# Kernel tuning notes

Hardware: AMD Instinct MI355X
Metric: run time of the kernel (lower is better)

## Reference

```python
import jax, jax.numpy as jnp
import numpy as np

N_NODES = 100000
N_EDGES = 1600000
D_IN = 128
D_HID = 128


def gcn_conv(x, src, dst, W, b, n_nodes):
    """PyG-style GCNConv: out = D^{-1/2} (A + I) D^{-1/2} (x @ W) + b.

    src/dst already include self-loops.
    """
    deg = jax.ops.segment_sum(jnp.ones_like(src, dtype=x.dtype), dst,
                              num_segments=n_nodes)
    dinv = jnp.where(deg > 0, deg ** -0.5, 0.0)
    norm = dinv[src] * dinv[dst]              # [E]
    h = x @ W                                  # [N, d_out]
    msg = h[src] * norm[:, None]               # gather + scale, [E, d_out]
    out = jax.ops.segment_sum(msg, dst, num_segments=n_nodes)
    return out + b


def setup_inputs() -> dict:
    key = jax.random.key(0)
    k1, k2, k3, k4 = jax.random.split(key, 4)
    x = jax.random.normal(k1, (N_NODES, D_IN), dtype=jnp.float32)
    edge_index = jax.random.randint(k2, (2, N_EDGES), 0, N_NODES, dtype=jnp.int64)
    s1 = (1.0 / np.sqrt(D_IN)).astype(np.float32)
    s2 = (1.0 / np.sqrt(D_HID)).astype(np.float32)
    W1 = jax.random.normal(k3, (D_IN, D_HID), dtype=jnp.float32) * s1
    b1 = jnp.zeros((D_HID,), dtype=jnp.float32)
    W2 = jax.random.normal(k4, (D_HID, D_HID), dtype=jnp.float32) * s2
    b2 = jnp.zeros((D_HID,), dtype=jnp.float32)
    return {"x": x, "edge_index": edge_index, "W1": W1, "b1": b1,
            "W2": W2, "b2": b2}


def reference(x, edge_index, W1, b1, W2, b2):
    n_nodes = x.shape[0]
    loops = jnp.arange(n_nodes, dtype=edge_index.dtype)
    src = jnp.concatenate([edge_index[0], loops])  # self-loops, as PyG default
    dst = jnp.concatenate([edge_index[1], loops])
    h = gcn_conv(x, src, dst, W1, b1, n_nodes)
    h = gcn_conv(h, src, dst, W2, b2, n_nodes)
    return h
```

## Files before the change

### kernel.cpp

```cpp
#include <hip/hip_runtime.h>

#define N_NODES 100000
#define N_EDGES 1600000

#define NBIN 196
#define BINCAP 9216
#define NPB 4096
#define EPT 16
#define BPT 36
#define PBLK ((N_EDGES + NPB - 1) / NPB)

typedef unsigned int uint;
typedef unsigned short u16;
typedef __attribute__((ext_vector_type(8))) short bf16x8;
typedef __attribute__((ext_vector_type(4))) float f32x4;

__device__ __forceinline__ uint bf16_rtne(float f) {
  uint u = __float_as_uint(f);
  return (u + 0x7fffu + ((u >> 16) & 1u)) >> 16;
}


__global__ __launch_bounds__(256) void k_zerobc(int* __restrict__ bin_cur) {
  if (threadIdx.x < NBIN) bin_cur[threadIdx.x] = 0;
}

__global__ __launch_bounds__(256) void k_part(const int* __restrict__ ei, int* __restrict__ bin_cur,
                                              uint* __restrict__ stage) {
  __shared__ uint hist[4][NBIN];
  __shared__ uint wbase[4][NBIN];
  __shared__ uint lcur[4][NBIN];
  const int t = threadIdx.x;
  const int w = t >> 6;
  const int e0 = blockIdx.x * NPB;
  for (int i = t; i < 4 * NBIN; i += 256) { (&hist[0][0])[i] = 0; (&lcur[0][0])[i] = 0; }
  __syncthreads();
  uint d[EPT];
#pragma unroll
  for (int j = 0; j < EPT; ++j) {
    int e = e0 + j * 256 + t;
    d[j] = (e < N_EDGES) ? (uint)ei[N_EDGES + e] : 0xFFFFFFFFu;
    if (d[j] != 0xFFFFFFFFu) atomicAdd(&hist[w][d[j] >> 9], 1u);
  }
  __syncthreads();
  if (t < NBIN) {
    uint h0 = hist[0][t], h1 = hist[1][t], h2 = hist[2][t], h3 = hist[3][t];
    uint tot = h0 + h1 + h2 + h3;
    uint g = tot ? (uint)atomicAdd(&bin_cur[t], (int)tot) : 0u;
    wbase[0][t] = g;
    wbase[1][t] = g + h0;
    wbase[2][t] = g + h0 + h1;
    wbase[3][t] = g + h0 + h1 + h2;
  }
  __syncthreads();
#pragma unroll
  for (int j = 0; j < EPT; ++j) {
    if (d[j] != 0xFFFFFFFFu) {
      int e = e0 + j * 256 + t;
      uint s = (uint)ei[e];
      uint b = d[j] >> 9;
      uint pos = wbase[w][b] + atomicAdd(&lcur[w][b], 1u);
      if (pos < BINCAP)
        stage[(size_t)b * BINCAP + pos] = s | ((d[j] & 511u) << 17);
    }
  }
}

__global__ __launch_bounds__(256) void k_binscan(const int* __restrict__ bin_cur,
                                                 int* __restrict__ ebase, int* __restrict__ rowptr) {
  __shared__ int sd[256];
  const int t = threadIdx.x;
  int v = (t < NBIN) ? min(bin_cur[t], BINCAP) : 0;
  int s = v;
  sd[t] = s;
  __syncthreads();
  for (int off = 1; off < 256; off <<= 1) {
    int a = (t >= off) ? sd[t - off] : 0;
    __syncthreads();
    sd[t] += a;
    __syncthreads();
  }
  if (t < NBIN) ebase[t] = sd[t] - v;
  if (t == 255) rowptr[N_NODES] = sd[255];
}

__global__ __launch_bounds__(256) void k_bin2(const int* __restrict__ bin_cur, const uint* __restrict__ stage,
                                              const int* __restrict__ ebase,
                                              float* __restrict__ dinv, int* __restrict__ rowptr,
                                              int* __restrict__ ep) {
  __shared__ int cnt[512];
  __shared__ int sd[256];
  __shared__ int curs[512];
  const int b = blockIdx.x, t = threadIdx.x;
  cnt[t] = 0; cnt[t + 256] = 0;
  __syncthreads();
  const int n = min(bin_cur[b], BINCAP);
  const uint* sb = stage + (size_t)b * BINCAP;
  uint r[BPT];
#pragma unroll
  for (int j = 0; j < BPT; ++j) {
    int i = j * 256 + t;
    r[j] = (i < n) ? sb[i] : 0xFFFFFFFFu;
  }
#pragma unroll
  for (int j = 0; j < BPT; ++j)
    if (r[j] != 0xFFFFFFFFu) atomicAdd(&cnt[r[j] >> 17], 1);
  __syncthreads();
  int v0 = cnt[t * 2], v1 = cnt[t * 2 + 1];
  int s = v0 + v1;
  sd[t] = s;
  __syncthreads();
  for (int off = 1; off < 256; off <<= 1) {
    int a = (t >= off) ? sd[t - off] : 0;
    __syncthreads();
    sd[t] += a;
    __syncthreads();
  }
  int run = sd[t] - s;
  int eb = ebase[b];
  int c0 = eb + run, c1 = eb + run + v0;
  int g0 = b * 512 + t * 2;
  if (g0 < N_NODES) {
    rowptr[g0] = c0;
    dinv[g0] = rsqrtf((float)(v0 + 1));
  }
  if (g0 + 1 < N_NODES) {
    rowptr[g0 + 1] = c1;
    dinv[g0 + 1] = rsqrtf((float)(v1 + 1));
  }
  curs[t * 2] = c0; curs[t * 2 + 1] = c1;
  __syncthreads();
#pragma unroll
  for (int j = 0; j < BPT; ++j)
    if (r[j] != 0xFFFFFFFFu) {
      int pos = atomicAdd(&curs[r[j] >> 17], 1);
      ep[pos] = (int)(r[j] & 0x1FFFFu);
    }
}


__global__ __launch_bounds__(256) void k_prepw(const float* __restrict__ W1, const float* __restrict__ W2,
                                               uint* __restrict__ S1, uint* __restrict__ S2) {
  int u = blockIdx.x * 256 + threadIdx.x;
  const float* W = blockIdx.y ? W2 : W1;
  uint* S = blockIdx.y ? S2 : S1;
  int lane = u & 63;
  int kcnt = u >> 6;
  int kc = kcnt & 3;
  int nt = kcnt >> 2;
  int n = nt * 16 + (lane & 15);
  int k0 = kc * 32 + (lane >> 4) * 8;
  float f[8];
#pragma unroll
  for (int j = 0; j < 8; ++j) f[j] = W[(size_t)(k0 + j) * 128 + n];
  uint4 pk;
  pk.x = bf16_rtne(f[0]) | (bf16_rtne(f[1]) << 16);
  pk.y = bf16_rtne(f[2]) | (bf16_rtne(f[3]) << 16);
  pk.z = bf16_rtne(f[4]) | (bf16_rtne(f[5]) << 16);
  pk.w = bf16_rtne(f[6]) | (bf16_rtne(f[7]) << 16);
  ((uint4*)S)[u] = pk;
}


__global__ __launch_bounds__(256) void k_gemm(const void* __restrict__ Ain, int a_f32,
                                              const uint* __restrict__ Wsw,
                                              u16* __restrict__ OutH, int nrows) {
  __shared__ uint As[4096];
  __shared__ uint Bs[8192];
  const int tid = threadIdx.x;
  const int R = blockIdx.x * 64;
  {
    const uint4* src = (const uint4*)Wsw;
    uint4* dst = (uint4*)Bs;
#pragma unroll
    for (int v = 0; v < 8; ++v) dst[tid + v * 256] = src[tid + v * 256];
  }
  const int unit = tid & 15;
  const int kc_s = unit >> 2;
  const int quad_s = unit & 3;
#pragma unroll
  for (int pass = 0; pass < 4; ++pass) {
    int row = pass * 16 + (tid >> 4);
    int gr = R + row;
    if (gr >= nrows) gr = nrows - 1;
    uint4 pk;
    if (a_f32) {
      const float* srcr = (const float*)Ain + (size_t)gr * 128 + unit * 8;
      float4 f0 = ((const float4*)srcr)[0];
      float4 f1 = ((const float4*)srcr)[1];
      pk.x = bf16_rtne(f0.x) | (bf16_rtne(f0.y) << 16);
      pk.y = bf16_rtne(f0.z) | (bf16_rtne(f0.w) << 16);
      pk.z = bf16_rtne(f1.x) | (bf16_rtne(f1.y) << 16);
      pk.w = bf16_rtne(f1.z) | (bf16_rtne(f1.w) << 16);
    } else {
      pk = ((const uint4*)((const uint*)Ain + (size_t)gr * 64))[unit];
    }
    int lane_t = quad_s * 16 + (row & 15);
    *(uint4*)&As[((pass * 4 + kc_s) * 64 + lane_t) * 4] = pk;
  }
  __syncthreads();

  const int w = tid >> 6;
  const int lane = tid & 63;
  bf16x8 a0 = *(bf16x8*)&As[((w * 4 + 0) * 64 + lane) * 4];
  bf16x8 a1 = *(bf16x8*)&As[((w * 4 + 1) * 64 + lane) * 4];
  bf16x8 a2 = *(bf16x8*)&As[((w * 4 + 2) * 64 + lane) * 4];
  bf16x8 a3 = *(bf16x8*)&As[((w * 4 + 3) * 64 + lane) * 4];
  f32x4 acc[8];
#pragma unroll
  for (int nt = 0; nt < 8; ++nt) acc[nt] = (f32x4){0.f, 0.f, 0.f, 0.f};
#pragma unroll
  for (int nt = 0; nt < 8; ++nt) {
    bf16x8 b0 = *(bf16x8*)&Bs[((nt * 4 + 0) * 64 + lane) * 4];
    bf16x8 b1 = *(bf16x8*)&Bs[((nt * 4 + 1) * 64 + lane) * 4];
    bf16x8 b2 = *(bf16x8*)&Bs[((nt * 4 + 2) * 64 + lane) * 4];
    bf16x8 b3 = *(bf16x8*)&Bs[((nt * 4 + 3) * 64 + lane) * 4];
    acc[nt] = __builtin_amdgcn_mfma_f32_16x16x32_bf16(a0, b0, acc[nt], 0, 0, 0);
    acc[nt] = __builtin_amdgcn_mfma_f32_16x16x32_bf16(a1, b1, acc[nt], 0, 0, 0);
    acc[nt] = __builtin_amdgcn_mfma_f32_16x16x32_bf16(a2, b2, acc[nt], 0, 0, 0);
    acc[nt] = __builtin_amdgcn_mfma_f32_16x16x32_bf16(a3, b3, acc[nt], 0, 0, 0);
  }
  const int colb = lane & 15;
  const int quad = lane >> 4;
#pragma unroll
  for (int nt = 0; nt < 8; ++nt) {
#pragma unroll
    for (int r = 0; r < 4; ++r) {
      int gr = R + w * 16 + quad * 4 + r;
      if (gr < nrows)
        OutH[(size_t)gr * 128 + nt * 16 + colb] = (u16)bf16_rtne(acc[nt][r]);
    }
  }
}


__device__ __forceinline__ void bacc(float& ax, float& ay, uint v, float w) {
  ax += w * __uint_as_float(v << 16);
  ay += w * __uint_as_float(v & 0xffff0000u);
}

__device__ __forceinline__ void agg_node(const uint* __restrict__ hb, const float* __restrict__ dinv,
                                         const int* __restrict__ ep, int node, int lane,
                                         int beg, int end, float dn, float& ax, float& ay) {
  uint selfv = hb[(size_t)node * 64 + lane];
  bacc(ax, ay, selfv, dn);
  int e = beg;
  for (; e + 8 <= end; e += 8) {
    int p[8];
#pragma unroll
    for (int j = 0; j < 8; ++j) p[j] = ep[e + j];
    float wt[8];
#pragma unroll
    for (int j = 0; j < 8; ++j) wt[j] = dinv[p[j]];
    uint v[8];
#pragma unroll
    for (int j = 0; j < 8; ++j) v[j] = hb[(size_t)p[j] * 64 + lane];
#pragma unroll
    for (int j = 0; j < 8; ++j) bacc(ax, ay, v[j], wt[j]);
  }
  if (e + 4 <= end) {
    int p[4];
#pragma unroll
    for (int j = 0; j < 4; ++j) p[j] = ep[e + j];
    float wt[4];
#pragma unroll
    for (int j = 0; j < 4; ++j) wt[j] = dinv[p[j]];
    uint v[4];
#pragma unroll
    for (int j = 0; j < 4; ++j) v[j] = hb[(size_t)p[j] * 64 + lane];
#pragma unroll
    for (int j = 0; j < 4; ++j) bacc(ax, ay, v[j], wt[j]);
    e += 4;
  }
  for (; e < end; ++e) {
    int p = ep[e];
    float wt = dinv[p];
    uint v = hb[(size_t)p * 64 + lane];
    bacc(ax, ay, v, wt);
  }
}


__global__ __launch_bounds__(256) void k_aggm(const uint* __restrict__ hb, const float* __restrict__ dinv,
                                              const int* __restrict__ rowptr, const int* __restrict__ ep,
                                              const float* __restrict__ bias, const uint* __restrict__ Wsw,
                                              u16* __restrict__ outH) {
  __shared__ uint Abf[16 * 64];
  const int w = threadIdx.x >> 6;
  const int lane = threadIdx.x & 63;
  const int nb = blockIdx.x * 16;
#pragma unroll 1
  for (int j = 0; j < 4; ++j) {
    const int lr = w * 4 + j;
    const int node = nb + lr;
    const int beg = rowptr[node];
    const int end = rowptr[node + 1];
    const float dn = dinv[node];
    float ax = 0.f, ay = 0.f;
    agg_node(hb, dinv, ep, node, lane, beg, end, dn, ax, ay);
    int c = lane * 2;
    float rx = dn * ax + bias[c];
    float ry = dn * ay + bias[c + 1];
    uint pk = bf16_rtne(rx) | (bf16_rtne(ry) << 16);
    Abf[(lr * 64 + lane) ^ ((lr & 7) << 2)] = pk;
  }
  __syncthreads();
  const int row = lane & 15;
  const int kq = lane >> 4;
  bf16x8 a[4];
#pragma unroll
  for (int kc = 0; kc < 4; ++kc) {
    int ui = row * 64 + kc * 16 + kq * 4;
    a[kc] = *(bf16x8*)&Abf[ui ^ ((row & 7) << 2)];
  }
  const int colb = lane & 15;
  const int quad = lane >> 4;
#pragma unroll
  for (int nt2 = 0; nt2 < 2; ++nt2) {
    const int nt = w * 2 + nt2;
    f32x4 acc = (f32x4){0.f, 0.f, 0.f, 0.f};
#pragma unroll
    for (int kc = 0; kc < 4; ++kc) {
      bf16x8 bfr = *(const bf16x8*)((const uint4*)Wsw + (nt * 4 + kc) * 64 + lane);
      acc = __builtin_amdgcn_mfma_f32_16x16x32_bf16(a[kc], bfr, acc, 0, 0, 0);
    }
#pragma unroll
    for (int r2 = 0; r2 < 4; ++r2) {
      int gr = nb + quad * 4 + r2;
      outH[(size_t)gr * 128 + nt * 16 + colb] = (u16)bf16_rtne(acc[r2]);
    }
  }
}


__global__ __launch_bounds__(256) void k_agg(const uint* __restrict__ hb, const float* __restrict__ dinv,
                                             const int* __restrict__ rowptr, const int* __restrict__ ep,
                                             const float* __restrict__ bias,
                                             float* __restrict__ outf) {
  int wid = threadIdx.x >> 6;
  int lane = threadIdx.x & 63;
  int node = blockIdx.x * 4 + wid;
  if (node >= N_NODES) return;
  int beg = rowptr[node];
  int end = rowptr[node + 1];
  float dn = dinv[node];
  float ax = 0.f, ay = 0.f;
  agg_node(hb, dinv, ep, node, lane, beg, end, dn, ax, ay);
  int c = lane * 2;
  float2 o;
  o.x = dn * ax + bias[c];
  o.y = dn * ay + bias[c + 1];
  *(float2*)(outf + (size_t)node * 128 + c) = o;
}


extern "C" void kernel_launch(void* const* d_in, const int* in_sizes, int n_in,
                              void* d_out, int out_size, void* d_ws, size_t ws_size,
                              hipStream_t stream) {
  const float* x  = (const float*)d_in[0];
  const int*   ei = (const int*)d_in[1];
  const float* W1 = (const float*)d_in[2];
  const float* b1 = (const float*)d_in[3];
  const float* W2 = (const float*)d_in[4];
  const float* b2 = (const float*)d_in[5];
  float* out = (float*)d_out;

  char* p = (char*)d_ws;
  uint*  hb     = (uint*)p;  p += (size_t)N_NODES * 64 * sizeof(uint);
  int*   ep     = (int*)p;   p += (size_t)N_EDGES * sizeof(int);
  uint*  wsw1   = (uint*)p;  p += 8192 * sizeof(uint);
  uint*  wsw2   = (uint*)p;  p += 8192 * sizeof(uint);
  float* dinv   = (float*)p; p += (size_t)N_NODES * sizeof(float);
  int*   rowptr = (int*)p;   p += (size_t)(N_NODES + 1) * sizeof(int);
  int*   bin_cur= (int*)p;   p += (size_t)NBIN * sizeof(int);
  int*   ebase  = (int*)p;   p += (size_t)NBIN * sizeof(int);
  p = (char*)(((uintptr_t)p + 63) & ~(uintptr_t)63);
  uint*  stage  = (uint*)p;
  uint*  hb2    = (uint*)p;

  const int GG = (N_NODES + 63) / 64;

  k_zerobc<<<1, 256, 0, stream>>>(bin_cur);
  k_part<<<PBLK, 256, 0, stream>>>(ei, bin_cur, stage);
  k_binscan<<<1, 256, 0, stream>>>(bin_cur, ebase, rowptr);
  k_bin2<<<NBIN, 256, 0, stream>>>(bin_cur, stage, ebase, dinv, rowptr, ep);
  k_prepw<<<dim3(8, 2), 256, 0, stream>>>(W1, W2, wsw1, wsw2);

  k_gemm<<<GG, 256, 0, stream>>>(x, 1, wsw1, (u16*)hb, N_NODES);
  k_aggm<<<N_NODES / 16, 256, 0, stream>>>(hb, dinv, rowptr, ep, b1, wsw2, (u16*)hb2);
  k_agg<<<(N_NODES + 3) / 4, 256, 0, stream>>>(hb2, dinv, rowptr, ep, b2, out);
}
```

Before: 319.0 us.

## Pack per-edge source dinv into edge list and use nontemporal loads/stores

Edge list becomes int2 pairs of (src index, dinv[src]), filled by a new k_epw kernel after binning. Both aggregation passes then skip the dependent gather of dinv per edge. Edge pairs are read, and outputs written, with nontemporal hints so they pollute the cache less. The trade is an extra kernel pass and twice the edge-array traffic in exchange for removing a random dependent load in the hot gather loops.

```diff
diff --git a/kernel.cpp b/kernel.cpp
--- a/kernel.cpp
+++ b/kernel.cpp
@@ -12,6 +12,7 @@
 
 typedef unsigned int uint;
 typedef unsigned short u16;
+typedef unsigned long long u64;
 typedef __attribute__((ext_vector_type(8))) short bf16x8;
 typedef __attribute__((ext_vector_type(4))) float f32x4;
 
@@ -87,7 +88,7 @@
 __global__ __launch_bounds__(256) void k_bin2(const int* __restrict__ bin_cur, const uint* __restrict__ stage,
                                               const int* __restrict__ ebase,
                                               float* __restrict__ dinv, int* __restrict__ rowptr,
-                                              int* __restrict__ ep) {
+                                              int2* __restrict__ ep) {
   __shared__ int cnt[512];
   __shared__ int sd[256];
   __shared__ int curs[512];
@@ -134,8 +135,18 @@
   for (int j = 0; j < BPT; ++j)
     if (r[j] != 0xFFFFFFFFu) {
       int pos = atomicAdd(&curs[r[j] >> 17], 1);
-      ep[pos] = (int)(r[j] & 0x1FFFFu);
-    }
+      int2 pr; pr.x = (int)(r[j] & 0x1FFFFu); pr.y = 0;
+      ep[pos] = pr;
+    }
+}
+
+__global__ __launch_bounds__(256) void k_epw(int2* __restrict__ ep, const float* __restrict__ dinv) {
+  int i = blockIdx.x * 256 + threadIdx.x;
+  if (i < N_EDGES) {
+    int2 v = ep[i];
+    v.y = __float_as_int(dinv[v.x]);
+    ep[i] = v;
+  }
 }
 
 
@@ -239,50 +250,47 @@
   ay += w * __uint_as_float(v & 0xffff0000u);
 }
 
-__device__ __forceinline__ void agg_node(const uint* __restrict__ hb, const float* __restrict__ dinv,
-                                         const int* __restrict__ ep, int node, int lane,
+__device__ __forceinline__ u64 nt_ld_pair(const int2* p) {
+  return __builtin_nontemporal_load((const u64*)p);
+}
+
+__device__ __forceinline__ void agg_node(const uint* __restrict__ hb, const int2* __restrict__ ep,
+                                         int node, int lane,
                                          int beg, int end, float dn, float& ax, float& ay) {
   uint selfv = hb[(size_t)node * 64 + lane];
   bacc(ax, ay, selfv, dn);
   int e = beg;
   for (; e + 8 <= end; e += 8) {
-    int p[8];
-#pragma unroll
-    for (int j = 0; j < 8; ++j) p[j] = ep[e + j];
-    float wt[8];
-#pragma unroll
-    for (int j = 0; j < 8; ++j) wt[j] = dinv[p[j]];
+    u64 p[8];
+#pragma unroll
+    for (int j = 0; j < 8; ++j) p[j] = nt_ld_pair(&ep[e + j]);
     uint v[8];
 #pragma unroll
-    for (int j = 0; j < 8; ++j) v[j] = hb[(size_t)p[j] * 64 + lane];
-#pragma unroll
-    for (int j = 0; j < 8; ++j) bacc(ax, ay, v[j], wt[j]);
+    for (int j = 0; j < 8; ++j) v[j] = hb[(size_t)(uint)p[j] * 64 + lane];
+#pragma unroll
+    for (int j = 0; j < 8; ++j) bacc(ax, ay, v[j], __uint_as_float((uint)(p[j] >> 32)));
   }
   if (e + 4 <= end) {
-    int p[4];
-#pragma unroll
-    for (int j = 0; j < 4; ++j) p[j] = ep[e + j];
-    float wt[4];
-#pragma unroll
-    for (int j = 0; j < 4; ++j) wt[j] = dinv[p[j]];
+    u64 p[4];
+#pragma unroll
+    for (int j = 0; j < 4; ++j) p[j] = nt_ld_pair(&ep[e + j]);
     uint v[4];
 #pragma unroll
-    for (int j = 0; j < 4; ++j) v[j] = hb[(size_t)p[j] * 64 + lane];
-#pragma unroll
-    for (int j = 0; j < 4; ++j) bacc(ax, ay, v[j], wt[j]);
+    for (int j = 0; j < 4; ++j) v[j] = hb[(size_t)(uint)p[j] * 64 + lane];
+#pragma unroll
+    for (int j = 0; j < 4; ++j) bacc(ax, ay, v[j], __uint_as_float((uint)(p[j] >> 32)));
     e += 4;
   }
   for (; e < end; ++e) {
-    int p = ep[e];
-    float wt = dinv[p];
-    uint v = hb[(size_t)p * 64 + lane];
-    bacc(ax, ay, v, wt);
+    u64 p = nt_ld_pair(&ep[e]);
+    uint v = hb[(size_t)(uint)p * 64 + lane];
+    bacc(ax, ay, v, __uint_as_float((uint)(p >> 32)));
   }
 }
 
 
 __global__ __launch_bounds__(256) void k_aggm(const uint* __restrict__ hb, const float* __restrict__ dinv,
-                                              const int* __restrict__ rowptr, const int* __restrict__ ep,
+                                              const int* __restrict__ rowptr, const int2* __restrict__ ep,
                                               const float* __restrict__ bias, const uint* __restrict__ Wsw,
                                               u16* __restrict__ outH) {
   __shared__ uint Abf[16 * 64];
@@ -297,7 +305,7 @@
     const int end = rowptr[node + 1];
     const float dn = dinv[node];
     float ax = 0.f, ay = 0.f;
-    agg_node(hb, dinv, ep, node, lane, beg, end, dn, ax, ay);
+    agg_node(hb, ep, node, lane, beg, end, dn, ax, ay);
     int c = lane * 2;
     float rx = dn * ax + bias[c];
     float ry = dn * ay + bias[c + 1];
@@ -327,14 +335,15 @@
 #pragma unroll
     for (int r2 = 0; r2 < 4; ++r2) {
       int gr = nb + quad * 4 + r2;
-      outH[(size_t)gr * 128 + nt * 16 + colb] = (u16)bf16_rtne(acc[r2]);
+      __builtin_nontemporal_store((u16)bf16_rtne(acc[r2]),
+                                  outH + (size_t)gr * 128 + nt * 16 + colb);
     }
   }
 }
 
 
 __global__ __launch_bounds__(256) void k_agg(const uint* __restrict__ hb, const float* __restrict__ dinv,
-                                             const int* __restrict__ rowptr, const int* __restrict__ ep,
+                                             const int* __restrict__ rowptr, const int2* __restrict__ ep,
                                              const float* __restrict__ bias,
                                              float* __restrict__ outf) {
   int wid = threadIdx.x >> 6;
@@ -345,12 +354,13 @@
   int end = rowptr[node + 1];
   float dn = dinv[node];
   float ax = 0.f, ay = 0.f;
-  agg_node(hb, dinv, ep, node, lane, beg, end, dn, ax, ay);
+  agg_node(hb, ep, node, lane, beg, end, dn, ax, ay);
   int c = lane * 2;
-  float2 o;
-  o.x = dn * ax + bias[c];
-  o.y = dn * ay + bias[c + 1];
-  *(float2*)(outf + (size_t)node * 128 + c) = o;
+  long long ov;
+  float rx = dn * ax + bias[c];
+  float ry = dn * ay + bias[c + 1];
+  ov = (long long)(((u64)__float_as_uint(ry) << 32) | (u64)__float_as_uint(rx));
+  __builtin_nontemporal_store(ov, (long long*)(outf + (size_t)node * 128 + c));
 }
 
 
@@ -367,7 +377,7 @@
 
   char* p = (char*)d_ws;
   uint*  hb     = (uint*)p;  p += (size_t)N_NODES * 64 * sizeof(uint);
-  int*   ep     = (int*)p;   p += (size_t)N_EDGES * sizeof(int);
+  int2*  ep     = (int2*)p;  p += (size_t)N_EDGES * sizeof(int2);
   uint*  wsw1   = (uint*)p;  p += 8192 * sizeof(uint);
   uint*  wsw2   = (uint*)p;  p += 8192 * sizeof(uint);
   float* dinv   = (float*)p; p += (size_t)N_NODES * sizeof(float);
@@ -384,6 +394,7 @@
   k_part<<<PBLK, 256, 0, stream>>>(ei, bin_cur, stage);
   k_binscan<<<1, 256, 0, stream>>>(bin_cur, ebase, rowptr);
   k_bin2<<<NBIN, 256, 0, stream>>>(bin_cur, stage, ebase, dinv, rowptr, ep);
+  k_epw<<<(N_EDGES + 255) / 256, 256, 0, stream>>>(ep, dinv);
   k_prepw<<<dim3(8, 2), 256, 0, stream>>>(W1, W2, wsw1, wsw2);
 
   k_gemm<<<GG, 256, 0, stream>>>(x, 1, wsw1, (u16*)hb, N_NODES);
```

Result: slower. 361.3 us (+13.3%).

## Merge partition and first GEMM into one launch and fold small kernels

Applied to the files above, without the earlier changes.

Edge partitioning and the layer-1 GEMM now run as one grid, with blocks branching by index, so the two independent stages overlap on the device. The bin counter reset moves into the weight-prep kernel, and the bin prefix scan is recomputed inside each k_bin2 block, which drops three small launches. This trades fewer launch gaps and better occupancy for a larger shared-memory footprint in the combined kernel and a redundant scan in every bin block.

```diff
diff --git a/kernel.cpp b/kernel.cpp
--- a/kernel.cpp
+++ b/kernel.cpp
@@ -9,9 +9,11 @@
 #define EPT 16
 #define BPT 36
 #define PBLK ((N_EDGES + NPB - 1) / NPB)
+#define GG ((N_NODES + 63) / 64)
 
 typedef unsigned int uint;
 typedef unsigned short u16;
+typedef unsigned long long u64;
 typedef __attribute__((ext_vector_type(8))) short bf16x8;
 typedef __attribute__((ext_vector_type(4))) float f32x4;
 
@@ -21,126 +23,10 @@
 }
 
 
-__global__ __launch_bounds__(256) void k_zerobc(int* __restrict__ bin_cur) {
-  if (threadIdx.x < NBIN) bin_cur[threadIdx.x] = 0;
-}
-
-__global__ __launch_bounds__(256) void k_part(const int* __restrict__ ei, int* __restrict__ bin_cur,
-                                              uint* __restrict__ stage) {
-  __shared__ uint hist[4][NBIN];
-  __shared__ uint wbase[4][NBIN];
-  __shared__ uint lcur[4][NBIN];
-  const int t = threadIdx.x;
-  const int w = t >> 6;
-  const int e0 = blockIdx.x * NPB;
-  for (int i = t; i < 4 * NBIN; i += 256) { (&hist[0][0])[i] = 0; (&lcur[0][0])[i] = 0; }
-  __syncthreads();
-  uint d[EPT];
-#pragma unroll
-  for (int j = 0; j < EPT; ++j) {
-    int e = e0 + j * 256 + t;
-    d[j] = (e < N_EDGES) ? (uint)ei[N_EDGES + e] : 0xFFFFFFFFu;
-    if (d[j] != 0xFFFFFFFFu) atomicAdd(&hist[w][d[j] >> 9], 1u);
-  }
-  __syncthreads();
-  if (t < NBIN) {
-    uint h0 = hist[0][t], h1 = hist[1][t], h2 = hist[2][t], h3 = hist[3][t];
-    uint tot = h0 + h1 + h2 + h3;
-    uint g = tot ? (uint)atomicAdd(&bin_cur[t], (int)tot) : 0u;
-    wbase[0][t] = g;
-    wbase[1][t] = g + h0;
-    wbase[2][t] = g + h0 + h1;
-    wbase[3][t] = g + h0 + h1 + h2;
-  }
-  __syncthreads();
-#pragma unroll
-  for (int j = 0; j < EPT; ++j) {
-    if (d[j] != 0xFFFFFFFFu) {
-      int e = e0 + j * 256 + t;
-      uint s = (uint)ei[e];
-      uint b = d[j] >> 9;
-      uint pos = wbase[w][b] + atomicAdd(&lcur[w][b], 1u);
-      if (pos < BINCAP)
-        stage[(size_t)b * BINCAP + pos] = s | ((d[j] & 511u) << 17);
-    }
-  }
-}
-
-__global__ __launch_bounds__(256) void k_binscan(const int* __restrict__ bin_cur,
-                                                 int* __restrict__ ebase, int* __restrict__ rowptr) {
-  __shared__ int sd[256];
-  const int t = threadIdx.x;
-  int v = (t < NBIN) ? min(bin_cur[t], BINCAP) : 0;
-  int s = v;
-  sd[t] = s;
-  __syncthreads();
-  for (int off = 1; off < 256; off <<= 1) {
-    int a = (t >= off) ? sd[t - off] : 0;
-    __syncthreads();
-    sd[t] += a;
-    __syncthreads();
-  }
-  if (t < NBIN) ebase[t] = sd[t] - v;
-  if (t == 255) rowptr[N_NODES] = sd[255];
-}
-
-__global__ __launch_bounds__(256) void k_bin2(const int* __restrict__ bin_cur, const uint* __restrict__ stage,
-                                              const int* __restrict__ ebase,
-                                              float* __restrict__ dinv, int* __restrict__ rowptr,
-                                              int* __restrict__ ep) {
-  __shared__ int cnt[512];
-  __shared__ int sd[256];
-  __shared__ int curs[512];
-  const int b = blockIdx.x, t = threadIdx.x;
-  cnt[t] = 0; cnt[t + 256] = 0;
-  __syncthreads();
-  const int n = min(bin_cur[b], BINCAP);
-  const uint* sb = stage + (size_t)b * BINCAP;
-  uint r[BPT];
-#pragma unroll
-  for (int j = 0; j < BPT; ++j) {
-    int i = j * 256 + t;
-    r[j] = (i < n) ? sb[i] : 0xFFFFFFFFu;
-  }
-#pragma unroll
-  for (int j = 0; j < BPT; ++j)
-    if (r[j] != 0xFFFFFFFFu) atomicAdd(&cnt[r[j] >> 17], 1);
-  __syncthreads();
-  int v0 = cnt[t * 2], v1 = cnt[t * 2 + 1];
-  int s = v0 + v1;
-  sd[t] = s;
-  __syncthreads();
-  for (int off = 1; off < 256; off <<= 1) {
-    int a = (t >= off) ? sd[t - off] : 0;
-    __syncthreads();
-    sd[t] += a;
-    __syncthreads();
-  }
-  int run = sd[t] - s;
-  int eb = ebase[b];
-  int c0 = eb + run, c1 = eb + run + v0;
-  int g0 = b * 512 + t * 2;
-  if (g0 < N_NODES) {
-    rowptr[g0] = c0;
-    dinv[g0] = rsqrtf((float)(v0 + 1));
-  }
-  if (g0 + 1 < N_NODES) {
-    rowptr[g0 + 1] = c1;
-    dinv[g0 + 1] = rsqrtf((float)(v1 + 1));
-  }
-  curs[t * 2] = c0; curs[t * 2 + 1] = c1;
-  __syncthreads();
-#pragma unroll
-  for (int j = 0; j < BPT; ++j)
-    if (r[j] != 0xFFFFFFFFu) {
-      int pos = atomicAdd(&curs[r[j] >> 17], 1);
-      ep[pos] = (int)(r[j] & 0x1FFFFu);
-    }
-}
-
-
 __global__ __launch_bounds__(256) void k_prepw(const float* __restrict__ W1, const float* __restrict__ W2,
-                                               uint* __restrict__ S1, uint* __restrict__ S2) {
+                                               uint* __restrict__ S1, uint* __restrict__ S2,
+                                               int* __restrict__ bin_cur) {
+  if (blockIdx.x == 0 && blockIdx.y == 0 && threadIdx.x < NBIN) bin_cur[threadIdx.x] = 0;
   int u = blockIdx.x * 256 + threadIdx.x;
   const float* W = blockIdx.y ? W2 : W1;
   uint* S = blockIdx.y ? S2 : S1;
@@ -162,13 +48,55 @@
 }
 
 
-__global__ __launch_bounds__(256) void k_gemm(const void* __restrict__ Ain, int a_f32,
-                                              const uint* __restrict__ Wsw,
-                                              u16* __restrict__ OutH, int nrows) {
-  __shared__ uint As[4096];
-  __shared__ uint Bs[8192];
+__device__ __forceinline__ void part_body(int bid, const int* __restrict__ ei,
+                                          int* __restrict__ bin_cur, uint* __restrict__ stage,
+                                          uint* smem) {
+  uint* hist  = smem;
+  uint* wbase = smem + 4 * NBIN;
+  uint* lcur  = smem + 8 * NBIN;
+  const int t = threadIdx.x;
+  const int w = t >> 6;
+  const int e0 = bid * NPB;
+  for (int i = t; i < 4 * NBIN; i += 256) { hist[i] = 0; lcur[i] = 0; }
+  __syncthreads();
+  uint d[EPT];
+#pragma unroll
+  for (int j = 0; j < EPT; ++j) {
+    int e = e0 + j * 256 + t;
+    d[j] = (e < N_EDGES) ? (uint)ei[N_EDGES + e] : 0xFFFFFFFFu;
+    if (d[j] != 0xFFFFFFFFu) atomicAdd(&hist[w * NBIN + (d[j] >> 9)], 1u);
+  }
+  __syncthreads();
+  if (t < NBIN) {
+    uint h0 = hist[t], h1 = hist[NBIN + t], h2 = hist[2 * NBIN + t], h3 = hist[3 * NBIN + t];
+    uint tot = h0 + h1 + h2 + h3;
+    uint g = tot ? (uint)atomicAdd(&bin_cur[t], (int)tot) : 0u;
+    wbase[t] = g;
+    wbase[NBIN + t] = g + h0;
+    wbase[2 * NBIN + t] = g + h0 + h1;
+    wbase[3 * NBIN + t] = g + h0 + h1 + h2;
+  }
+  __syncthreads();
+#pragma unroll
+  for (int j = 0; j < EPT; ++j) {
+    if (d[j] != 0xFFFFFFFFu) {
+      int e = e0 + j * 256 + t;
+      uint s = (uint)ei[e];
+      uint b = d[j] >> 9;
+      uint pos = wbase[w * NBIN + b] + atomicAdd(&lcur[w * NBIN + b], 1u);
+      if (pos < BINCAP)
+        stage[(size_t)b * BINCAP + pos] = s | ((d[j] & 511u) << 17);
+    }
+  }
+}
+
+__device__ __forceinline__ void gemm_body(int gb, const float* __restrict__ x,
+                                          const uint* __restrict__ Wsw, u16* __restrict__ OutH,
+                                          uint* smem) {
+  uint* As = smem;
+  uint* Bs = smem + 4096;
   const int tid = threadIdx.x;
-  const int R = blockIdx.x * 64;
+  const int R = gb * 64;
   {
     const uint4* src = (const uint4*)Wsw;
     uint4* dst = (uint4*)Bs;
@@ -182,19 +110,15 @@
   for (int pass = 0; pass < 4; ++pass) {
     int row = pass * 16 + (tid >> 4);
     int gr = R + row;
-    if (gr >= nrows) gr = nrows - 1;
+    if (gr >= N_NODES) gr = N_NODES - 1;
+    const float* srcr = x + (size_t)gr * 128 + unit * 8;
+    float4 f0 = ((const float4*)srcr)[0];
+    float4 f1 = ((const float4*)srcr)[1];
     uint4 pk;
-    if (a_f32) {
-      const float* srcr = (const float*)Ain + (size_t)gr * 128 + unit * 8;
-      float4 f0 = ((const float4*)srcr)[0];
-      float4 f1 = ((const float4*)srcr)[1];
-      pk.x = bf16_rtne(f0.x) | (bf16_rtne(f0.y) << 16);
-      pk.y = bf16_rtne(f0.z) | (bf16_rtne(f0.w) << 16);
-      pk.z = bf16_rtne(f1.x) | (bf16_rtne(f1.y) << 16);
-      pk.w = bf16_rtne(f1.z) | (bf16_rtne(f1.w) << 16);
-    } else {
-      pk = ((const uint4*)((const uint*)Ain + (size_t)gr * 64))[unit];
-    }
+    pk.x = bf16_rtne(f0.x) | (bf16_rtne(f0.y) << 16);
+    pk.y = bf16_rtne(f0.z) | (bf16_rtne(f0.w) << 16);
+    pk.z = bf16_rtne(f1.x) | (bf16_rtne(f1.y) << 16);
+    pk.w = bf16_rtne(f1.z) | (bf16_rtne(f1.w) << 16);
     int lane_t = quad_s * 16 + (row & 15);
     *(uint4*)&As[((pass * 4 + kc_s) * 64 + lane_t) * 4] = pk;
   }
@@ -227,10 +151,85 @@
 #pragma unroll
     for (int r = 0; r < 4; ++r) {
       int gr = R + w * 16 + quad * 4 + r;
-      if (gr < nrows)
+      if (gr < N_NODES)
         OutH[(size_t)gr * 128 + nt * 16 + colb] = (u16)bf16_rtne(acc[nt][r]);
     }
   }
+}
+
+__global__ __launch_bounds__(256) void k_pg(const int* __restrict__ ei, int* __restrict__ bin_cur,
+                                            uint* __restrict__ stage,
+                                            const float* __restrict__ x, const uint* __restrict__ Wsw,
+                                            u16* __restrict__ OutH) {
+  __shared__ uint smem[12288];
+  if ((int)blockIdx.x < PBLK) part_body(blockIdx.x, ei, bin_cur, stage, smem);
+  else                        gemm_body(blockIdx.x - PBLK, x, Wsw, OutH, smem);
+}
+
+
+__global__ __launch_bounds__(256) void k_bin2(const int* __restrict__ bin_cur, const uint* __restrict__ stage,
+                                              float* __restrict__ dinv, int* __restrict__ rowptr,
+                                              int* __restrict__ ep) {
+  __shared__ int cnt[512];
+  __shared__ int sd[256];
+  __shared__ int curs[512];
+  const int b = blockIdx.x, t = threadIdx.x;
+  int vg = (t < NBIN) ? min(bin_cur[t], BINCAP) : 0;
+  sd[t] = vg;
+  __syncthreads();
+  for (int off = 1; off < 256; off <<= 1) {
+    int a = (t >= off) ? sd[t - off] : 0;
+    __syncthreads();
+    sd[t] += a;
+    __syncthreads();
+  }
+  const int eb = (b > 0) ? sd[b - 1] : 0;
+  if (b == 0 && t == 0) rowptr[N_NODES] = sd[NBIN - 1];
+  __syncthreads();
+
+  cnt[t] = 0; cnt[t + 256] = 0;
+  __syncthreads();
+  const int n = min(bin_cur[b], BINCAP);
+  const uint* sb = stage + (size_t)b * BINCAP;
+  uint r[BPT];
+#pragma unroll
+  for (int j = 0; j < BPT; ++j) {
+    int i = j * 256 + t;
+    r[j] = (i < n) ? sb[i] : 0xFFFFFFFFu;
+  }
+#pragma unroll
+  for (int j = 0; j < BPT; ++j)
+    if (r[j] != 0xFFFFFFFFu) atomicAdd(&cnt[r[j] >> 17], 1);
+  __syncthreads();
+  int v0 = cnt[t * 2], v1 = cnt[t * 2 + 1];
+  int s = v0 + v1;
+  sd[t] = s;
+  __syncthreads();
+  for (int off = 1; off < 256; off <<= 1) {
+    int a = (t >= off) ? sd[t - off] : 0;
+    __syncthreads();
+    sd[t] += a;
+    __syncthreads();
+  }
+  int run = sd[t] - s;
+  int c0 = eb + run, c1 = eb + run + v0;
+  int g0 = b * 512 + t * 2;
+  if (g0 < N_NODES) {
+    rowptr[g0] = c0;
+    dinv[g0] = rsqrtf((float)(v0 + 1));
+  }
+  if (g0 + 1 < N_NODES) {
+    rowptr[g0 + 1] = c1;
+    dinv[g0 + 1] = rsqrtf((float)(v1 + 1));
+  }
+  curs[t * 2] = c0; curs[t * 2 + 1] = c1;
+  __syncthreads();
+#pragma unroll
+  for (int j = 0; j < BPT; ++j)
+    if (r[j] != 0xFFFFFFFFu) {
+      int pos = atomicAdd(&curs[r[j] >> 17], 1);
+      ep[pos] = (int)(r[j] & 0x1FFFFu);
+    }
 }
 
 
@@ -373,20 +372,13 @@
   float* dinv   = (float*)p; p += (size_t)N_NODES * sizeof(float);
   int*   rowptr = (int*)p;   p += (size_t)(N_NODES + 1) * sizeof(int);
   int*   bin_cur= (int*)p;   p += (size_t)NBIN * sizeof(int);
-  int*   ebase  = (int*)p;   p += (size_t)NBIN * sizeof(int);
-  p = (char*)(((uintptr_t)p + 63) & ~(uintptr_t)63);
+  p = (char*)(((uintptr_t)p + 255) & ~(uintptr_t)255);
   uint*  stage  = (uint*)p;
   uint*  hb2    = (uint*)p;
 
-  const int GG = (N_NODES + 63) / 64;
-
-  k_zerobc<<<1, 256, 0, stream>>>(bin_cur);
-  k_part<<<PBLK, 256, 0, stream>>>(ei, bin_cur, stage);
-  k_binscan<<<1, 256, 0, stream>>>(bin_cur, ebase, rowptr);
-  k_bin2<<<NBIN, 256, 0, stream>>>(bin_cur, stage, ebase, dinv, rowptr, ep);
-  k_prepw<<<dim3(8, 2), 256, 0, stream>>>(W1, W2, wsw1, wsw2);
-
-  k_gemm<<<GG, 256, 0, stream>>>(x, 1, wsw1, (u16*)hb, N_NODES);
+  k_prepw<<<dim3(8, 2), 256, 0, stream>>>(W1, W2, wsw1, wsw2, bin_cur);
+  k_pg<<<PBLK + GG, 256, 0, stream>>>(ei, bin_cur, stage, x, wsw1, (u16*)hb);
+  k_bin2<<<NBIN, 256, 0, stream>>>(bin_cur, stage, dinv, rowptr, ep);
   k_aggm<<<N_NODES / 16, 256, 0, stream>>>(hb, dinv, rowptr, ep, b1, wsw2, (u16*)hb2);
   k_agg<<<(N_NODES + 3) / 4, 256, 0, stream>>>(hb2, dinv, rowptr, ep, b2, out);
 }
```

Measured after the change: 292.3 us. 8.4% less time.
